# Performance work log

Measured on AMD Instinct MI355X. Metric: run time of the kernel, lower is better.

Reference implementation:

```python
import jax, jax.numpy as jnp
import numpy as np

INPUT_SIZE = 512
HIDDEN_SIZE = 1024
OUTPUT_SIZE = 2
SEQ_LENGTH = 64
BATCH = 2048


def setup_inputs() -> dict:
    key = jax.random.key(0)
    ks = jax.random.split(key, 9)
    cin = INPUT_SIZE + HIDDEN_SIZE
    s = 1.0 / np.sqrt(cin)
    x = jax.random.normal(ks[0], (BATCH, SEQ_LENGTH, INPUT_SIZE), dtype=jnp.float32)
    Wf = jax.random.uniform(ks[1], (HIDDEN_SIZE, cin), jnp.float32, -s, s)
    bf = jax.random.uniform(ks[2], (HIDDEN_SIZE,), jnp.float32, -s, s)
    Wg = jax.random.uniform(ks[3], (HIDDEN_SIZE, cin), jnp.float32, -s, s)
    bg = jax.random.uniform(ks[4], (HIDDEN_SIZE,), jnp.float32, -s, s)
    Wh = jax.random.uniform(ks[5], (HIDDEN_SIZE, cin), jnp.float32, -s, s)
    bh = jax.random.uniform(ks[6], (HIDDEN_SIZE,), jnp.float32, -s, s)
    sf = 1.0 / np.sqrt(HIDDEN_SIZE)
    Wfc = jax.random.uniform(ks[7], (OUTPUT_SIZE, HIDDEN_SIZE), jnp.float32, -sf, sf)
    bfc = jax.random.uniform(ks[8], (OUTPUT_SIZE,), jnp.float32, -sf, sf)
    return {"x": x, "Wf": Wf, "bf": bf, "Wg": Wg, "bg": bg,
            "Wh": Wh, "bh": bh, "Wfc": Wfc, "bfc": bfc}


def _lnn_forward(x, Wf, bf, Wg, bg, Wh, bh, Wfc, bfc):
    B = x.shape[0]
    h0 = jnp.zeros((B, Wf.shape[0]), dtype=x.dtype)
    xs = jnp.swapaxes(x, 0, 1)  # [T, B, D]

    def step(h, xt):
        combined = jnp.concatenate([xt, h], axis=-1)  # [B, D+H]
        f_out = combined @ Wf.T + bf
        g_out = combined @ Wg.T + bg
        h_out = combined @ Wh.T + bh
        gate = jax.nn.sigmoid(-f_out)
        new_h = gate * g_out + (1.0 - gate) * h_out
        return new_h, None

    h_final, _ = jax.lax.scan(step, h0, xs)
    return h_final @ Wfc.T + bfc  # [B, output_size]


def reference(x, Wf, bf, Wg, bg, Wh, bh, Wfc, bfc):
    return _lnn_forward(x, Wf, bf, Wg, bg, Wh, bh, Wfc, bfc)
```

## Files before the change

### kernel.cpp

```cpp
#include <hip/hip_runtime.h>

#define BATCH 2048
#define TSEQ  64
#define DIN   512
#define HID   1024
#define CIN   1536

#define BM 128
#define BN 32
#define BK 64
#define KITERS (CIN / BK)

#define CHUNK   1088
#define A_CHUNKS 16
#define B_CHUNKS 4
#define A_BYTES (A_CHUNKS * CHUNK)
#define B_MAT   (B_CHUNKS * CHUNK)
#define BUF_BYTES (A_BYTES + 3 * B_MAT)

typedef __attribute__((ext_vector_type(8))) short bf16x8;
typedef __attribute__((ext_vector_type(4))) float f32x4;
typedef __attribute__((ext_vector_type(4))) float fvec4;
typedef __attribute__((ext_vector_type(4))) unsigned int uvec4;

__device__ __forceinline__ unsigned short f2bf(float f) {
    unsigned int u = __float_as_uint(f);
    u += 0x7fffu + ((u >> 16) & 1u);
    return (unsigned short)(u >> 16);
}
__device__ __forceinline__ float bf2f(unsigned short u) {
    return __uint_as_float(((unsigned int)u) << 16);
}

__device__ __forceinline__ void gload_lds16(const void* g, void* lds) {
    __builtin_amdgcn_global_load_lds(
        (const __attribute__((address_space(1))) void*)(uintptr_t)g,
        (__attribute__((address_space(3))) void*)(unsigned)(uintptr_t)lds,
        16, 0, 0);
}

__global__ __launch_bounds__(256) void convert_w(const float* __restrict__ Wf,
                                                 const float* __restrict__ Wg,
                                                 const float* __restrict__ Wh,
                                                 unsigned short* __restrict__ Wb) {
    int mat = blockIdx.y;
    const float* src = (mat == 0) ? Wf : ((mat == 1) ? Wg : Wh);
    size_t base = (size_t)mat * (size_t)(HID * CIN);
    size_t idx = ((size_t)blockIdx.x * 256 + threadIdx.x) * 8;
    const fvec4* s = (const fvec4*)(src + idx);
    fvec4 a = s[0], b = s[1];
    uvec4 o;
    o.x = (unsigned)f2bf(a.x) | ((unsigned)f2bf(a.y) << 16);
    o.y = (unsigned)f2bf(a.z) | ((unsigned)f2bf(a.w) << 16);
    o.z = (unsigned)f2bf(b.x) | ((unsigned)f2bf(b.y) << 16);
    o.w = (unsigned)f2bf(b.z) | ((unsigned)f2bf(b.w) << 16);
    *(uvec4*)(Wb + base + idx) = o;
}

__global__ __launch_bounds__(256) void convert_x(const float* __restrict__ x,
                                                 unsigned short* __restrict__ xb) {
    size_t e = ((size_t)blockIdx.x * 256 + threadIdx.x) * 8;
    int t   = (int)(e / ((size_t)BATCH * DIN));
    int rem = (int)(e % ((size_t)BATCH * DIN));
    int b = rem / DIN;
    int d = rem % DIN;
    const float* src = x + ((size_t)b * TSEQ + t) * DIN + d;
    fvec4 a = *(const fvec4*)src;
    fvec4 c = *(const fvec4*)(src + 4);
    uvec4 o;
    o.x = (unsigned)f2bf(a.x) | ((unsigned)f2bf(a.y) << 16);
    o.y = (unsigned)f2bf(a.z) | ((unsigned)f2bf(a.w) << 16);
    o.z = (unsigned)f2bf(c.x) | ((unsigned)f2bf(c.y) << 16);
    o.w = (unsigned)f2bf(c.z) | ((unsigned)f2bf(c.w) << 16);
    *(uvec4*)(xb + e) = o;
}

__global__ __launch_bounds__(256, 2) void step_kernel(
    const unsigned short* __restrict__ xb,
    const unsigned short* __restrict__ Wb,
    const float* __restrict__ bfv,
    const float* __restrict__ bgv,
    const float* __restrict__ bhv,
    const unsigned short* __restrict__ hin,
    unsigned short* __restrict__ hout,
    int t)
{
    __shared__ __align__(16) char lds[2][BUF_BYTES];

    const int tid  = threadIdx.x;
    const int bid  = blockIdx.x;
    const int n_tile = ((bid & 7) << 2) | ((bid >> 3) & 3);
    const int m_tile = bid >> 5;
    const int m0 = m_tile * BM;
    const int n0 = n_tile * BN;

    const int lane = tid & 63;
    const int wave = tid >> 6;
    const int wm = wave >> 1;
    const int wn = wave & 1;

    const int drow = lane >> 3;
    const int dcol = (lane & 7) * 8;

    f32x4 acc[3][4] = {};

    const int cg = n0 + wn * 16 + (lane & 15);
    const float biasF = bfv[cg];
    const float biasG = bgv[cg];
    const float biasH = bhv[cg];

    const unsigned short* xsrc = xb + (size_t)t * BATCH * DIN;

    int aoff[4];
#pragma unroll
    for (int mt = 0; mt < 4; ++mt) {
        int r = wm * 64 + mt * 16 + (lane & 15);
        aoff[mt] = (r >> 3) * CHUNK + (r & 7) * 128;
    }
    const int nloc = wn * 16 + (lane & 15);
    const int boff = (nloc >> 3) * CHUNK + (nloc & 7) * 128;
    const int kboff = (lane >> 4) * 16;

    auto stage = [&](int ki, int bb) {
        char* base = lds[bb];
        const int k0 = ki * BK;
        const unsigned short* asrc;
        int astride;
        if (k0 < DIN) { asrc = xsrc + k0;        astride = DIN; }
        else          { asrc = hin + (k0 - DIN); astride = HID; }
#pragma unroll
        for (int c = 0; c < 4; ++c) {
            int chunk = wave * 4 + c;
            gload_lds16(asrc + (size_t)(m0 + chunk * 8 + drow) * astride + dcol,
                        base + chunk * CHUNK);
        }
#pragma unroll
        for (int j = 0; j < 3; ++j) {
            int u = wave * 3 + j;
            int mat = u >> 2, chunk = u & 3;
            gload_lds16(Wb + (size_t)mat * (HID * CIN) + (size_t)(n0 + chunk * 8 + drow) * CIN
                           + k0 + dcol,
                        base + A_BYTES + mat * B_MAT + chunk * CHUNK);
        }
    };

    auto compute = [&](int bb) {
        const char* base = lds[bb];
#pragma unroll
        for (int ks = 0; ks < 2; ++ks) {
            const int kb = ks * 64 + kboff;
            bf16x8 af[4];
#pragma unroll
            for (int mt = 0; mt < 4; ++mt)
                af[mt] = *(const bf16x8*)(base + aoff[mt] + kb);
#pragma unroll
            for (int mat = 0; mat < 3; ++mat) {
                bf16x8 bq = *(const bf16x8*)(base + A_BYTES + mat * B_MAT + boff + kb);
#pragma unroll
                for (int mt = 0; mt < 4; ++mt)
                    acc[mat][mt] = __builtin_amdgcn_mfma_f32_16x16x32_bf16(
                        af[mt], bq, acc[mat][mt], 0, 0, 0);
            }
        }
    };

    stage(0, 0);
    for (int ki = 0; ki < KITERS; ++ki) {
        const int bb = ki & 1;
        __syncthreads();
        if (ki < KITERS - 1) stage(ki + 1, bb ^ 1);
        compute(bb);
    }

#pragma unroll
    for (int mt = 0; mt < 4; ++mt) {
        int rbase = m0 + wm * 64 + mt * 16 + (lane >> 4) * 4;
#pragma unroll
        for (int r = 0; r < 4; ++r) {
            float f  = acc[0][mt][r] + biasF;
            float g  = acc[1][mt][r] + biasG;
            float hh = acc[2][mt][r] + biasH;
            float gate = 1.0f / (1.0f + __expf(f));
            float nh = hh + gate * (g - hh);
            __builtin_nontemporal_store(f2bf(nh),
                hout + (size_t)(rbase + r) * HID + cg);
        }
    }
}

__global__ __launch_bounds__(256) void fc_kernel(const unsigned short* __restrict__ h,
                                                 const float* __restrict__ Wfc,
                                                 const float* __restrict__ bfc,
                                                 float* __restrict__ out) {
    int row = blockIdx.x;
    int tid = threadIdx.x;
    const unsigned short* hr = h + (size_t)row * HID;
    ushort4 hv = *(const ushort4*)(hr + tid * 4);
    float h0 = bf2f(hv.x), h1 = bf2f(hv.y), h2 = bf2f(hv.z), h3 = bf2f(hv.w);
    float4 w0 = *(const float4*)(Wfc + tid * 4);
    float4 w1 = *(const float4*)(Wfc + HID + tid * 4);
    float a0 = h0 * w0.x + h1 * w0.y + h2 * w0.z + h3 * w0.w;
    float a1 = h0 * w1.x + h1 * w1.y + h2 * w1.z + h3 * w1.w;
#pragma unroll
    for (int off = 32; off > 0; off >>= 1) {
        a0 += __shfl_down(a0, off);
        a1 += __shfl_down(a1, off);
    }
    __shared__ float red[2][4];
    if ((tid & 63) == 0) { red[0][tid >> 6] = a0; red[1][tid >> 6] = a1; }
    __syncthreads();
    if (tid == 0) out[(size_t)row * 2 + 0] = red[0][0] + red[0][1] + red[0][2] + red[0][3] + bfc[0];
    if (tid == 1) out[(size_t)row * 2 + 1] = red[1][0] + red[1][1] + red[1][2] + red[1][3] + bfc[1];
}

extern "C" void kernel_launch(void* const* d_in, const int* in_sizes, int n_in,
                              void* d_out, int out_size, void* d_ws, size_t ws_size,
                              hipStream_t stream) {
    const float* x   = (const float*)d_in[0];
    const float* Wf  = (const float*)d_in[1];
    const float* bfv = (const float*)d_in[2];
    const float* Wg  = (const float*)d_in[3];
    const float* bgv = (const float*)d_in[4];
    const float* Wh  = (const float*)d_in[5];
    const float* bhv = (const float*)d_in[6];
    const float* Wfc = (const float*)d_in[7];
    const float* bfc = (const float*)d_in[8];
    float* out = (float*)d_out;

    char* ws = (char*)d_ws;
    unsigned short* Wb = (unsigned short*)ws;
    size_t wb_bytes = (size_t)3 * HID * CIN * 2;
    size_t h_bytes  = (size_t)BATCH * HID * 2;
    unsigned short* h0 = (unsigned short*)(ws + wb_bytes);
    unsigned short* h1 = (unsigned short*)(ws + wb_bytes + h_bytes);
    unsigned short* xbuf = (unsigned short*)(ws + wb_bytes + 2 * h_bytes);

    convert_w<<<dim3(768, 3), 256, 0, stream>>>(Wf, Wg, Wh, Wb);
    convert_x<<<32768, 256, 0, stream>>>(x, xbuf);
    (void)hipMemsetAsync(h0, 0, h_bytes, stream);

    unsigned short* bufs[2] = {h0, h1};
    for (int t = 0; t < TSEQ; ++t) {
        step_kernel<<<512, 256, 0, stream>>>(xbuf, Wb, bfv, bgv, bhv,
                                             bufs[t & 1], bufs[(t + 1) & 1], t);
    }
    fc_kernel<<<BATCH, 256, 0, stream>>>(h0, Wfc, bfc, out);
}
```

Before: 2.029 ms.

## Fuse all recurrent timesteps into one persistent kernel with a grid barrier

Replaces the 64 per-timestep kernel launches with a single persistent kernel of 512 blocks. The kernel loops over timesteps, ping-pongs the hidden-state buffers, and synchronises all blocks through a two-level atomic grid barrier: eight sub-counters feed one master counter. Before waiting at the barrier, each block prefetches the next step's first x tile into shared memory, overlapping that load with the barrier wait. This removes per-launch overhead and kernel tail gaps. It relies on all 512 blocks being co-resident and adds the cost of spinning on the barrier.

```diff
diff --git a/kernel.cpp b/kernel.cpp
--- a/kernel.cpp
+++ b/kernel.cpp
@@ -1,4 +1,5 @@
 #include <hip/hip_runtime.h>
+#include <stdint.h>
 
 #define BATCH 2048
 #define TSEQ  64
@@ -10,6 +11,7 @@
 #define BN 32
 #define BK 64
 #define KITERS (CIN / BK)
+#define NBLOCKS 512
 
 #define CHUNK   1088
 #define A_CHUNKS 16
@@ -75,15 +77,15 @@
     *(uvec4*)(xb + e) = o;
 }
 
-__global__ __launch_bounds__(256, 2) void step_kernel(
+__global__ __launch_bounds__(256, 2) void lnn_steps(
     const unsigned short* __restrict__ xb,
     const unsigned short* __restrict__ Wb,
     const float* __restrict__ bfv,
     const float* __restrict__ bgv,
     const float* __restrict__ bhv,
-    const unsigned short* __restrict__ hin,
-    unsigned short* __restrict__ hout,
-    int t)
+    unsigned short* __restrict__ hA,
+    unsigned short* __restrict__ hB,
+    unsigned* bar)
 {
     __shared__ __align__(16) char lds[2][BUF_BYTES];
 
@@ -102,14 +104,10 @@
     const int drow = lane >> 3;
     const int dcol = (lane & 7) * 8;
 
-    f32x4 acc[3][4] = {};
-
     const int cg = n0 + wn * 16 + (lane & 15);
     const float biasF = bfv[cg];
     const float biasG = bgv[cg];
     const float biasH = bhv[cg];
-
-    const unsigned short* xsrc = xb + (size_t)t * BATCH * DIN;
 
     int aoff[4];
 #pragma unroll
@@ -121,8 +119,7 @@
     const int boff = (nloc >> 3) * CHUNK + (nloc & 7) * 128;
     const int kboff = (lane >> 4) * 16;
 
-    auto stage = [&](int ki, int bb) {
-        char* base = lds[bb];
+    auto stage = [&](int ki, char* base, const unsigned short* xsrc, const unsigned short* hin) {
         const int k0 = ki * BK;
         const unsigned short* asrc;
         int astride;
@@ -144,46 +141,72 @@
         }
     };
 
-    auto compute = [&](int bb) {
-        const char* base = lds[bb];
-#pragma unroll
-        for (int ks = 0; ks < 2; ++ks) {
-            const int kb = ks * 64 + kboff;
-            bf16x8 af[4];
-#pragma unroll
-            for (int mt = 0; mt < 4; ++mt)
-                af[mt] = *(const bf16x8*)(base + aoff[mt] + kb);
-#pragma unroll
-            for (int mat = 0; mat < 3; ++mat) {
-                bf16x8 bq = *(const bf16x8*)(base + A_BYTES + mat * B_MAT + boff + kb);
+    stage(0, lds[0], xb, hA);
+
+    for (int t = 0; t < TSEQ; ++t) {
+        const unsigned short* xsrc = xb + (size_t)t * BATCH * DIN;
+        const unsigned short* hin  = (t & 1) ? hB : hA;
+        unsigned short*       hout = (t & 1) ? hA : hB;
+
+        f32x4 acc[3][4] = {};
+
+        for (int ki = 0; ki < KITERS; ++ki) {
+            const int bb = ki & 1;
+            __syncthreads();
+            if (ki < KITERS - 1) stage(ki + 1, lds[bb ^ 1], xsrc, hin);
+            const char* base = lds[bb];
+#pragma unroll
+            for (int ks = 0; ks < 2; ++ks) {
+                const int kb = ks * 64 + kboff;
+                bf16x8 af[4];
 #pragma unroll
                 for (int mt = 0; mt < 4; ++mt)
-                    acc[mat][mt] = __builtin_amdgcn_mfma_f32_16x16x32_bf16(
-                        af[mt], bq, acc[mat][mt], 0, 0, 0);
+                    af[mt] = *(const bf16x8*)(base + aoff[mt] + kb);
+#pragma unroll
+                for (int mat = 0; mat < 3; ++mat) {
+                    bf16x8 bq = *(const bf16x8*)(base + A_BYTES + mat * B_MAT + boff + kb);
+#pragma unroll
+                    for (int mt = 0; mt < 4; ++mt)
+                        acc[mat][mt] = __builtin_amdgcn_mfma_f32_16x16x32_bf16(
+                            af[mt], bq, acc[mat][mt], 0, 0, 0);
+                }
             }
         }
-    };
-
-    stage(0, 0);
-    for (int ki = 0; ki < KITERS; ++ki) {
-        const int bb = ki & 1;
-        __syncthreads();
-        if (ki < KITERS - 1) stage(ki + 1, bb ^ 1);
-        compute(bb);
-    }
-
-#pragma unroll
-    for (int mt = 0; mt < 4; ++mt) {
-        int rbase = m0 + wm * 64 + mt * 16 + (lane >> 4) * 4;
-#pragma unroll
-        for (int r = 0; r < 4; ++r) {
-            float f  = acc[0][mt][r] + biasF;
-            float g  = acc[1][mt][r] + biasG;
-            float hh = acc[2][mt][r] + biasH;
-            float gate = 1.0f / (1.0f + __expf(f));
-            float nh = hh + gate * (g - hh);
-            __builtin_nontemporal_store(f2bf(nh),
-                hout + (size_t)(rbase + r) * HID + cg);
+
+#pragma unroll
+        for (int mt = 0; mt < 4; ++mt) {
+            int rbase = m0 + wm * 64 + mt * 16 + (lane >> 4) * 4;
+#pragma unroll
+            for (int r = 0; r < 4; ++r) {
+                float f  = acc[0][mt][r] + biasF;
+                float g  = acc[1][mt][r] + biasG;
+                float hh = acc[2][mt][r] + biasH;
+                float gate = 1.0f / (1.0f + __expf(f));
+                float nh = hh + gate * (g - hh);
+                __builtin_nontemporal_store(f2bf(nh),
+                    hout + (size_t)(rbase + r) * HID + cg);
+            }
+        }
+
+        if (t + 1 < TSEQ) {
+            __syncthreads();
+            stage(0, lds[0], xsrc + (size_t)BATCH * DIN, hin);
+            if (tid == 0) {
+                __threadfence();
+                unsigned* sub    = bar + ((bid & 7) << 5);
+                unsigned* master = bar + 256;
+                unsigned a = __hip_atomic_fetch_add(sub, 1u, __ATOMIC_ACQ_REL,
+                                                    __HIP_MEMORY_SCOPE_AGENT);
+                if (a == (unsigned)(t + 1) * (NBLOCKS / 8) - 1u)
+                    __hip_atomic_fetch_add(master, 1u, __ATOMIC_ACQ_REL,
+                                           __HIP_MEMORY_SCOPE_AGENT);
+                const unsigned mtarget = (unsigned)(t + 1) * 8u;
+                while (__hip_atomic_load(master, __ATOMIC_RELAXED,
+                                         __HIP_MEMORY_SCOPE_AGENT) < mtarget)
+                    __builtin_amdgcn_s_sleep(2);
+                __threadfence();
+            }
+            __syncthreads();
         }
     }
 }
@@ -231,18 +254,17 @@
     unsigned short* Wb = (unsigned short*)ws;
     size_t wb_bytes = (size_t)3 * HID * CIN * 2;
     size_t h_bytes  = (size_t)BATCH * HID * 2;
+    size_t xb_bytes = (size_t)TSEQ * BATCH * DIN * 2;
     unsigned short* h0 = (unsigned short*)(ws + wb_bytes);
     unsigned short* h1 = (unsigned short*)(ws + wb_bytes + h_bytes);
     unsigned short* xbuf = (unsigned short*)(ws + wb_bytes + 2 * h_bytes);
+    unsigned* bar = (unsigned*)(ws + wb_bytes + 2 * h_bytes + xb_bytes);
 
     convert_w<<<dim3(768, 3), 256, 0, stream>>>(Wf, Wg, Wh, Wb);
     convert_x<<<32768, 256, 0, stream>>>(x, xbuf);
     (void)hipMemsetAsync(h0, 0, h_bytes, stream);
-
-    unsigned short* bufs[2] = {h0, h1};
-    for (int t = 0; t < TSEQ; ++t) {
-        step_kernel<<<512, 256, 0, stream>>>(xbuf, Wb, bfv, bgv, bhv,
-                                             bufs[t & 1], bufs[(t + 1) & 1], t);
-    }
+    (void)hipMemsetAsync(bar, 0, 2048, stream);
+
+    lnn_steps<<<NBLOCKS, 256, 0, stream>>>(xbuf, Wb, bfv, bgv, bhv, h0, h1, bar);
     fc_kernel<<<BATCH, 256, 0, stream>>>(h0, Wfc, bfc, out);
 }
```

After: 4.115 ms. +102.9%, slower.

## Load weight fragments directly into registers, bypassing LDS staging

Applied to the files above, without the earlier changes.

The weight (B) operand tiles are no longer staged through shared memory. Each lane now loads its MFMA B fragments straight from global memory into registers, prefetching the next K-step one iteration ahead. This removes the LDS traffic and footprint for the three weight matrices, which could raise occupancy, at the cost of more vector registers and uncoalesced-ish 16-byte global loads per lane with exposed latency.

```diff
diff --git a/kernel.cpp b/kernel.cpp
--- a/kernel.cpp
+++ b/kernel.cpp
@@ -1,4 +1,5 @@
 #include <hip/hip_runtime.h>
+#include <stdint.h>
 
 #define BATCH 2048
 #define TSEQ  64
@@ -13,10 +14,7 @@
 
 #define CHUNK   1088
 #define A_CHUNKS 16
-#define B_CHUNKS 4
 #define A_BYTES (A_CHUNKS * CHUNK)
-#define B_MAT   (B_CHUNKS * CHUNK)
-#define BUF_BYTES (A_BYTES + 3 * B_MAT)
 
 typedef __attribute__((ext_vector_type(8))) short bf16x8;
 typedef __attribute__((ext_vector_type(4))) float f32x4;
@@ -85,7 +83,7 @@
     unsigned short* __restrict__ hout,
     int t)
 {
-    __shared__ __align__(16) char lds[2][BUF_BYTES];
+    __shared__ __align__(16) char lds[2][A_BYTES];
 
     const int tid  = threadIdx.x;
     const int bid  = blockIdx.x;
@@ -117,9 +115,19 @@
         int r = wm * 64 + mt * 16 + (lane & 15);
         aoff[mt] = (r >> 3) * CHUNK + (r & 7) * 128;
     }
-    const int nloc = wn * 16 + (lane & 15);
-    const int boff = (nloc >> 3) * CHUNK + (nloc & 7) * 128;
     const int kboff = (lane >> 4) * 16;
+
+    const unsigned short* wbase[3];
+#pragma unroll
+    for (int mat = 0; mat < 3; ++mat)
+        wbase[mat] = Wb + (size_t)mat * (HID * CIN) + (size_t)cg * CIN + ((lane >> 4) * 8);
+
+    bf16x8 bq[3][2];
+#pragma unroll
+    for (int mat = 0; mat < 3; ++mat)
+#pragma unroll
+        for (int ks = 0; ks < 2; ++ks)
+            bq[mat][ks] = *(const bf16x8*)(wbase[mat] + ks * 32);
 
     auto stage = [&](int ki, int bb) {
         char* base = lds[bb];
@@ -134,42 +142,44 @@
             gload_lds16(asrc + (size_t)(m0 + chunk * 8 + drow) * astride + dcol,
                         base + chunk * CHUNK);
         }
-#pragma unroll
-        for (int j = 0; j < 3; ++j) {
-            int u = wave * 3 + j;
-            int mat = u >> 2, chunk = u & 3;
-            gload_lds16(Wb + (size_t)mat * (HID * CIN) + (size_t)(n0 + chunk * 8 + drow) * CIN
-                           + k0 + dcol,
-                        base + A_BYTES + mat * B_MAT + chunk * CHUNK);
-        }
-    };
-
-    auto compute = [&](int bb) {
-        const char* base = lds[bb];
-#pragma unroll
-        for (int ks = 0; ks < 2; ++ks) {
-            const int kb = ks * 64 + kboff;
-            bf16x8 af[4];
-#pragma unroll
-            for (int mt = 0; mt < 4; ++mt)
-                af[mt] = *(const bf16x8*)(base + aoff[mt] + kb);
-#pragma unroll
-            for (int mat = 0; mat < 3; ++mat) {
-                bf16x8 bq = *(const bf16x8*)(base + A_BYTES + mat * B_MAT + boff + kb);
-#pragma unroll
-                for (int mt = 0; mt < 4; ++mt)
-                    acc[mat][mt] = __builtin_amdgcn_mfma_f32_16x16x32_bf16(
-                        af[mt], bq, acc[mat][mt], 0, 0, 0);
-            }
-        }
     };
 
     stage(0, 0);
     for (int ki = 0; ki < KITERS; ++ki) {
         const int bb = ki & 1;
         __syncthreads();
-        if (ki < KITERS - 1) stage(ki + 1, bb ^ 1);
-        compute(bb);
+        bf16x8 bqn[3][2];
+        if (ki < KITERS - 1) {
+            const int k0n = (ki + 1) * BK;
+#pragma unroll
+            for (int mat = 0; mat < 3; ++mat)
+#pragma unroll
+                for (int ks = 0; ks < 2; ++ks)
+                    bqn[mat][ks] = *(const bf16x8*)(wbase[mat] + k0n + ks * 32);
+            stage(ki + 1, bb ^ 1);
+        }
+        const char* base = lds[bb];
+#pragma unroll
+        for (int ks = 0; ks < 2; ++ks) {
+            const int kb = ks * 64 + kboff;
+            bf16x8 af[4];
+#pragma unroll
+            for (int mt = 0; mt < 4; ++mt)
+                af[mt] = *(const bf16x8*)(base + aoff[mt] + kb);
+#pragma unroll
+            for (int mat = 0; mat < 3; ++mat)
+#pragma unroll
+                for (int mt = 0; mt < 4; ++mt)
+                    acc[mat][mt] = __builtin_amdgcn_mfma_f32_16x16x32_bf16(
+                        af[mt], bq[mat][ks], acc[mat][mt], 0, 0, 0);
+        }
+        if (ki < KITERS - 1) {
+#pragma unroll
+            for (int mat = 0; mat < 3; ++mat)
+#pragma unroll
+                for (int ks = 0; ks < 2; ++ks)
+                    bq[mat][ks] = bqn[mat][ks];
+        }
     }
 
 #pragma unroll
```

Result: slower. 3.060 ms (+50.9%).

## Triple-buffer activation tiles and prefetch two stages ahead with partial vmcnt waits

Applied to the files above, without the earlier changes.

Splits shared memory into separate A (activation) and B (weight) buffers, with A triple-buffered and loaded two K-steps ahead while B stays double-buffered. The main loop is unrolled and uses an explicit s_waitcnt vmcnt(4) plus s_barrier instead of __syncthreads, so the latest A prefetch stays in flight while computing. It aims to hide global-to-LDS latency further, at the cost of more LDS per block (possibly limiting occupancy) and larger code from full unrolling. It relies on the load issue order matching the hand-chosen wait count.

```diff
diff --git a/kernel.cpp b/kernel.cpp
--- a/kernel.cpp
+++ b/kernel.cpp
@@ -1,4 +1,5 @@
 #include <hip/hip_runtime.h>
+#include <stdint.h>
 
 #define BATCH 2048
 #define TSEQ  64
@@ -16,7 +17,7 @@
 #define B_CHUNKS 4
 #define A_BYTES (A_CHUNKS * CHUNK)
 #define B_MAT   (B_CHUNKS * CHUNK)
-#define BUF_BYTES (A_BYTES + 3 * B_MAT)
+#define B_BYTES (3 * B_MAT)
 
 typedef __attribute__((ext_vector_type(8))) short bf16x8;
 typedef __attribute__((ext_vector_type(4))) float f32x4;
@@ -85,7 +86,8 @@
     unsigned short* __restrict__ hout,
     int t)
 {
-    __shared__ __align__(16) char lds[2][BUF_BYTES];
+    __shared__ __align__(16) char ldsA[3][A_BYTES];
+    __shared__ __align__(16) char ldsB[2][B_BYTES];
 
     const int tid  = threadIdx.x;
     const int bid  = blockIdx.x;
@@ -121,8 +123,7 @@
     const int boff = (nloc >> 3) * CHUNK + (nloc & 7) * 128;
     const int kboff = (lane >> 4) * 16;
 
-    auto stage = [&](int ki, int bb) {
-        char* base = lds[bb];
+    auto stageA = [&](int ki, char* base) {
         const int k0 = ki * BK;
         const unsigned short* asrc;
         int astride;
@@ -134,28 +135,29 @@
             gload_lds16(asrc + (size_t)(m0 + chunk * 8 + drow) * astride + dcol,
                         base + chunk * CHUNK);
         }
+    };
+    auto stageB = [&](int ki, char* base) {
+        const int k0 = ki * BK;
 #pragma unroll
         for (int j = 0; j < 3; ++j) {
             int u = wave * 3 + j;
             int mat = u >> 2, chunk = u & 3;
             gload_lds16(Wb + (size_t)mat * (HID * CIN) + (size_t)(n0 + chunk * 8 + drow) * CIN
                            + k0 + dcol,
-                        base + A_BYTES + mat * B_MAT + chunk * CHUNK);
+                        base + mat * B_MAT + chunk * CHUNK);
         }
     };
-
-    auto compute = [&](int bb) {
-        const char* base = lds[bb];
+    auto compute = [&](const char* baseA, const char* baseB) {
 #pragma unroll
         for (int ks = 0; ks < 2; ++ks) {
             const int kb = ks * 64 + kboff;
             bf16x8 af[4];
 #pragma unroll
             for (int mt = 0; mt < 4; ++mt)
-                af[mt] = *(const bf16x8*)(base + aoff[mt] + kb);
+                af[mt] = *(const bf16x8*)(baseA + aoff[mt] + kb);
 #pragma unroll
             for (int mat = 0; mat < 3; ++mat) {
-                bf16x8 bq = *(const bf16x8*)(base + A_BYTES + mat * B_MAT + boff + kb);
+                bf16x8 bq = *(const bf16x8*)(baseB + mat * B_MAT + boff + kb);
 #pragma unroll
                 for (int mt = 0; mt < 4; ++mt)
                     acc[mat][mt] = __builtin_amdgcn_mfma_f32_16x16x32_bf16(
@@ -164,13 +166,19 @@
         }
     };
 
-    stage(0, 0);
-    for (int ki = 0; ki < KITERS; ++ki) {
-        const int bb = ki & 1;
-        __syncthreads();
-        if (ki < KITERS - 1) stage(ki + 1, bb ^ 1);
-        compute(bb);
-    }
+    stageA(0, ldsA[0]);
+    stageB(0, ldsB[0]);
+    stageA(1, ldsA[1]);
+
+#pragma unroll
+    for (int p = 0; p < KITERS - 1; ++p) {
+        asm volatile("s_waitcnt vmcnt(4) lgkmcnt(0)\n\ts_barrier" ::: "memory");
+        stageB(p + 1, ldsB[(p + 1) & 1]);
+        if (p + 2 < KITERS) stageA(p + 2, ldsA[(p + 2) % 3]);
+        compute(ldsA[p % 3], ldsB[p & 1]);
+    }
+    asm volatile("s_waitcnt vmcnt(0) lgkmcnt(0)\n\ts_barrier" ::: "memory");
+    compute(ldsA[(KITERS - 1) % 3], ldsB[(KITERS - 1) & 1]);
 
 #pragma unroll
     for (int mt = 0; mt < 4; ++mt) {
```

After: 1.874 ms. 7.6% less time.
